# Performance work log

Measured on AMD Instinct MI355X. Metric: run time of the kernel, lower is better.

The kernel has to match this reference:

```python
import jax, jax.numpy as jnp
import numpy as np

SIGMA = 10
POPULATIONS = 2
LR = 0.001


def _normalize(L, prior):
    # clamp then normalize over populations (logsumexp across the population axis)
    O = L.shape[1]
    L = jnp.clip(L, -5.0, 0.0)
    lse = jax.nn.logsumexp(L.reshape(POPULATIONS, -1, O), axis=0)  # (in/P, O)
    L = L - jnp.tile(lse, (POPULATIONS, 1))
    prior = jnp.clip(prior, -5.0, 0.0)
    prior = prior - jax.nn.logsumexp(prior)
    return L, prior


def _forward(x, L, prior):
    B, T, IN = x.shape
    O = L.shape[1]
    L, prior = _normalize(L, prior)  # matches normalize_probs() in __init__

    # membrane potential: OR of spikes over trailing window of SIGMA steps
    xb = x.astype(bool)
    pot = xb
    for s in range(1, SIGMA):  # fixed small loop (sigma=10)
        pot = pot | jnp.pad(xb, ((0, 0), (s, 0), (0, 0)))[:, :T, :]

    tpre0 = jnp.full((B, IN), -T, dtype=jnp.int32)
    tpost0 = jnp.full((B, O), jnp.iinfo(jnp.int32).max, dtype=jnp.int32)
    base_key = jax.random.key(42)

    pot_T = jnp.transpose(pot, (1, 0, 2))  # (T,B,IN)
    x_T = jnp.transpose(xb, (1, 0, 2))

    def step(carry, inp):
        L, prior, tpre, tpost, t = carry
        pot_t, x_t = inp
        potf = pot_t.astype(L.dtype)
        logits = potf @ L + prior  # (B,O), logits <= 0 so exp is safe
        # torch: softmax(exp(logits)).multinomial == categorical with logits=exp(logits)
        key = jax.random.fold_in(base_key, t)
        widx = jax.random.categorical(key, jnp.exp(logits), axis=-1)  # (B,)
        win = jax.nn.one_hot(widx, O, dtype=L.dtype)
        # trace updates happen BEFORE STDP, as in the torch code
        tpre = jnp.where(x_t, 0, tpre - 1)
        tpost = jnp.where(win > 0, 0, tpost - 1)
        ltp = (tpre >= -SIGMA).astype(L.dtype)
        ltd = (tpre < -SIGMA).astype(L.dtype)
        post = (tpost < 0).astype(L.dtype)
        m_ltp = jnp.einsum('bi,bo->io', ltp, win) / B
        m_ltd = jnp.einsum('bi,bo->io', ltd, win) / B
        m_pp = jnp.einsum('bi,bo->io', potf, post) / B
        decay = (t + 1).astype(L.dtype)  # lr_decay_inverse starts at 1
        # dw = (5 e^{-L} - 1) * LTP.mean - LTD.mean - pre_post.mean ; LTD was negated
        dw = (5.0 * jnp.exp(-L) - 1.0) * m_ltp + m_ltd - m_pp
        L2 = L + (LR / decay) * dw
        wm = jnp.mean(win, axis=0)
        db = (-5.0 * prior - 1.0) * wm - (1.0 - wm)
        p2 = prior + (LR / decay) * db
        L2, p2 = _normalize(L2, p2)
        return (L2, p2, tpre, tpost, t + 1), None

    (Lf, pf, _, _, _), _ = jax.lax.scan(
        step, (L, prior, tpre0, tpost0, jnp.int32(0)), (pot_T, x_T))
    return jnp.concatenate([Lf.reshape(-1), pf])


def setup_inputs() -> dict:
    key = jax.random.key(0)
    k1, k2, k3 = jax.random.split(key, 3)
    B, T, IN, O = 256, 200, 1568, 100
    x = jax.random.randint(k1, (B, T, IN), 0, 2, dtype=jnp.int32)
    log_likelihood = jax.random.uniform(k2, (IN, O), dtype=jnp.float32) * -1.0 - 1.0
    log_prior = jax.random.uniform(k3, (O,), dtype=jnp.float32) * -1.0 - 1.0
    return {"x": x, "log_likelihood": log_likelihood, "log_prior": log_prior}


def reference(x, log_likelihood, log_prior):
    return _forward(x, log_likelihood, log_prior)
```

## Files before the change

kernel.cpp:

```cpp
#include <hip/hip_runtime.h>
#include <stdint.h>

#define BB 256
#define TT 200
#define INN 1568
#define OO 100
#define PAIRS 784
#define NHALF 12800
#define NBLK 240
#define UNITS 686
#define ROWSTRIDE (4 * INN)

typedef unsigned long long u64;
typedef __attribute__((ext_vector_type(4))) int v4i;

typedef const __attribute__((address_space(1))) uint32_t* gas_p;
typedef __attribute__((address_space(3))) uint32_t* las_p;
#define GLD16(g, l) __builtin_amdgcn_global_load_lds((gas_p)(g), (las_p)(l), 16, 0, 0)

__device__ __forceinline__ void tf_round(uint32_t& x0, uint32_t& x1, int r) {
    x0 += x1;
    x1 = (x1 << r) | (x1 >> (32 - r));
    x1 ^= x0;
}

__device__ __forceinline__ void threefry(uint32_t k0, uint32_t k1,
                                         uint32_t x0, uint32_t x1,
                                         uint32_t& o0, uint32_t& o1) {
    uint32_t k2 = k0 ^ k1 ^ 0x1BD11BDAu;
    x0 += k0; x1 += k1;
    tf_round(x0,x1,13); tf_round(x0,x1,15); tf_round(x0,x1,26); tf_round(x0,x1,6);
    x0 += k1; x1 += k2 + 1u;
    tf_round(x0,x1,17); tf_round(x0,x1,29); tf_round(x0,x1,16); tf_round(x0,x1,24);
    x0 += k2; x1 += k0 + 2u;
    tf_round(x0,x1,13); tf_round(x0,x1,15); tf_round(x0,x1,26); tf_round(x0,x1,6);
    x0 += k0; x1 += k1 + 3u;
    tf_round(x0,x1,17); tf_round(x0,x1,29); tf_round(x0,x1,16); tf_round(x0,x1,24);
    x0 += k1; x1 += k2 + 4u;
    tf_round(x0,x1,13); tf_round(x0,x1,15); tf_round(x0,x1,26); tf_round(x0,x1,6);
    o0 = x0 + k2; o1 = x1 + k0 + 5u;
}

struct FusedSM {
    u64 rows[8][16][64];
    u64 wp[8][8][128];
    u64 potC[8][2][8][10];
    u64 ltpC[8][2][8][10];
    uint32_t cntR[8][8][16];
};
struct FwSM { uint32_t wl32[TT * 65]; int fwl[BB]; };
union SMem { FusedSM f; FwSM w; };

__device__ __forceinline__ void gridsync(uint32_t* c) {
    __syncthreads();
    if (threadIdx.x == 0) {
        __threadfence();
        __hip_atomic_fetch_add(c, 1u, __ATOMIC_ACQ_REL, __HIP_MEMORY_SCOPE_AGENT);
        while (__hip_atomic_load(c, __ATOMIC_ACQUIRE, __HIP_MEMORY_SCOPE_AGENT)
               < (uint32_t)NBLK)
            __builtin_amdgcn_s_sleep(8);
        __threadfence();
    }
    __syncthreads();
}

__global__ __launch_bounds__(512, 1) void k_mono(
        const int* __restrict__ x,
        const float* __restrict__ L0,
        const float* __restrict__ p0arr,
        uint32_t* __restrict__ syncc,
        uint8_t* __restrict__ widx,
        uint32_t* __restrict__ cntg,
        u64* __restrict__ winbits,
        u64* __restrict__ postbits,
        u64* __restrict__ bitB,
        float* __restrict__ outL,
        float* __restrict__ outp) {
    __shared__ SMem sm;
    __shared__ uint32_t smclaim;
    const int tid = threadIdx.x;
    const int bid = blockIdx.x;

    {
        int idx = bid * 214 + tid;
        if (tid < 214 && idx < TT * BB) {
            int t = idx >> 8, b = idx & 255;
            uint32_t fk0, fk1;
            threefry(0u, 42u, 0u, (uint32_t)t, fk0, fk1);
            uint32_t bestkey = 0u;
            int bo = 0;
            int nbase = b * OO;
            for (int o = 0; o < OO; ++o) {
                uint32_t n = (uint32_t)(nbase + o);
                uint32_t lo = (n < NHALF) ? n : n - NHALF;
                uint32_t v0, v1;
                threefry(fk0, fk1, lo, lo + NHALF, v0, v1);
                uint32_t bits = (n < NHALF) ? v0 : v1;
                uint32_t key = bits >> 9;
                if (key > bestkey) { bestkey = key; bo = o; }
            }
            widx[idx] = (uint8_t)bo;
        }
    }
    gridsync(&syncc[0]);

    if (bid < 100) {
        const uint32_t* wsrc = (const uint32_t*)widx;
        for (int g = tid; g < TT * 64; g += 512)
            sm.w.wl32[(g >> 6) * 65 + (g & 63)] = wsrc[g];
        __syncthreads();
        int o = bid;
        if (tid < 64) {
            int f0 = 255, f1 = 255, f2 = 255, f3 = 255;
            for (int t = 0; t < TT; ++t) {
                uint32_t w4 = sm.w.wl32[t * 65 + tid];
                if (((w4      ) & 255u) == (uint32_t)o && f0 == 255) f0 = t;
                if (((w4 >>  8) & 255u) == (uint32_t)o && f1 == 255) f1 = t;
                if (((w4 >> 16) & 255u) == (uint32_t)o && f2 == 255) f2 = t;
                if (((w4 >> 24) & 255u) == (uint32_t)o && f3 == 255) f3 = t;
            }
            sm.w.fwl[4 * tid + 0] = f0; sm.w.fwl[4 * tid + 1] = f1;
            sm.w.fwl[4 * tid + 2] = f2; sm.w.fwl[4 * tid + 3] = f3;
        }
        __syncthreads();
        if (tid < TT) {
            int t = tid;
            u64 wbA[4], pbA[4];
            uint32_t c = 0;
            #pragma unroll
            for (int k = 0; k < 4; ++k) {
                u64 wacc = 0, pacc = 0;
                for (int q2 = 0; q2 < 16; ++q2) {
                    uint32_t w4 = sm.w.wl32[t * 65 + k * 16 + q2];
                    #pragma unroll
                    for (int j = 0; j < 4; ++j) {
                        int bl = q2 * 4 + j;
                        bool win = (((w4 >> (8 * j)) & 255u) == (uint32_t)o);
                        c += win ? 1u : 0u;
                        bool post = (sm.w.fwl[k * 64 + q2 * 4 + j] < t) && !win;
                        u64 bit = 1ull << bl;
                        if (win)  wacc |= bit;
                        if (post) pacc |= bit;
                    }
                }
                wbA[k] = wacc; pbA[k] = pacc;
            }
            size_t base = (size_t)(t * OO + o) * 4;
            #pragma unroll
            for (int k = 0; k < 4; ++k) {
                winbits[base + k] = wbA[k];
                postbits[base + k] = pbA[k];
            }
            cntg[t * OO + o] = c;
        }
        __syncthreads();
    }

    {
        const v4i* xp = (const v4i*)x;
        for (;;) {
            __syncthreads();
            if (tid == 0)
                smclaim = __hip_atomic_fetch_add(&syncc[2], 1u, __ATOMIC_RELAXED,
                                                 __HIP_MEMORY_SCOPE_AGENT);
            __syncthreads();
            uint32_t u = smclaim;
            if (u >= 200u) break;
            int wb = u & 3, tc = u >> 2;
            u64 acc[4][4];
            #pragma unroll
            for (int q = 0; q < 4; ++q)
                #pragma unroll
                for (int c = 0; c < 4; ++c) acc[q][c] = 0;
            bool x4 = (tid < 32);
            for (int blb = 0; blb < 64; blb += 4) {
                v4i v[4][3];
                v4i vt[4];
                #pragma unroll
                for (int s4 = 0; s4 < 4; ++s4) {
                    size_t base = ((size_t)((wb * 64 + blb + s4) * TT + tc * 4)) * 392;
                    #pragma unroll
                    for (int q = 0; q < 3; ++q)
                        v[s4][q] = __builtin_nontemporal_load(&xp[base + tid + q * 512]);
                    if (x4)
                        vt[s4] = __builtin_nontemporal_load(&xp[base + tid + 1536]);
                }
                #pragma unroll
                for (int s4 = 0; s4 < 4; ++s4) {
                    u64 bit = 1ull << (blb + s4);
                    #pragma unroll
                    for (int q = 0; q < 3; ++q) {
                        if (v[s4][q].x) acc[q][0] |= bit;
                        if (v[s4][q].y) acc[q][1] |= bit;
                        if (v[s4][q].z) acc[q][2] |= bit;
                        if (v[s4][q].w) acc[q][3] |= bit;
                    }
                    if (x4) {
                        if (vt[s4].x) acc[3][0] |= bit;
                        if (vt[s4].y) acc[3][1] |= bit;
                        if (vt[s4].z) acc[3][2] |= bit;
                        if (vt[s4].w) acc[3][3] |= bit;
                    }
                }
            }
            #pragma unroll
            for (int q = 0; q < 4; ++q) {
                if (q == 3 && !x4) continue;
                int p = tid + q * 512;
                int tp = (p >= 1176) ? 3 : (p >= 784) ? 2 : (p >= 392) ? 1 : 0;
                int iq = p - tp * 392;
                u64* dst = bitB + ((size_t)((tc * 4 + tp) * 4 + wb)) * INN + iq * 4;
                dst[0] = acc[q][0]; dst[1] = acc[q][1];
                dst[2] = acc[q][2]; dst[3] = acc[q][3];
            }
        }
    }
    gridsync(&syncc[1]);

    {
        const int wv = tid >> 6, lane = tid & 63;
        int u = bid + NBLK * wv;
        if (u > UNITS) return;
        if (u == UNITS) {
            int l = lane;
            bool has2 = (l + 64) < OO;
            float pa = p0arr[l];
            float pb = has2 ? p0arr[l + 64] : -1e30f;
            auto norm = [&]() {
                pa = fminf(fmaxf(pa, -5.0f), 0.0f);
                if (has2) pb = fminf(fmaxf(pb, -5.0f), 0.0f);
                float mx = has2 ? fmaxf(pa, pb) : pa;
                #pragma unroll
                for (int s = 32; s > 0; s >>= 1) mx = fmaxf(mx, __shfl_xor(mx, s, 64));
                float smv = expf(pa - mx) + (has2 ? expf(pb - mx) : 0.0f);
                #pragma unroll
                for (int s = 32; s > 0; s >>= 1) smv += __shfl_xor(smv, s, 64);
                float lse = logf(smv) + mx;
                pa -= lse;
                if (has2) pb -= lse;
            };
            norm();
            for (int t = 0; t < TT; ++t) {
                float eta = 0.001f / (float)(t + 1);
                float wma = (float)cntg[t * OO + l] * (1.0f / 256.0f);
                pa += eta * ((-5.0f * pa - 1.0f) * wma - (1.0f - wma));
                if (has2) {
                    float wmb = (float)cntg[t * OO + l + 64] * (1.0f / 256.0f);
                    pb += eta * ((-5.0f * pb - 1.0f) * wmb - (1.0f - wmb));
                }
                norm();
            }
            outp[l] = pa;
            if (has2) outp[l + 64] = pb;
            return;
        }

        const int pg = u % 98, og = u / 98;
        const int p0 = pg * 8, o0 = og * 16;
        const int pl = lane & 7, ol = lane >> 3;
        const int oA = o0 + ol, oB = oA + 8;
        const int i0 = p0 + pl, i1 = i0 + PAIRS;
        const bool actA = (oA < OO), actB = (oB < OO);

        const int e0 = (lane & 31) * 2;
        const int wk0 = e0 >> 3, wpl0 = e0 & 7;
        const u64* rowg = bitB + (size_t)((wk0 & 3) * INN + (wk0 >> 2) * PAIRS
                                          + p0 + wpl0);
        const int lw = lane & 31;
        const u64* wpg = (lane < 32) ? winbits : postbits;
        const bool wpact = (o0 + (lw >> 1)) < OO;
        const bool cntact = (lane < 8) && ((o0 + (lane & 3) * 4) < OO);

        auto issueG = [&](int G) {
            int r0 = 2 * G;
            {
                int rr = r0 + (lane >> 5); if (rr > TT - 1) rr = TT - 1;
                GLD16(rowg + (size_t)rr * ROWSTRIDE,
                      (las_p)&sm.f.rows[wv][r0 & 15][0]);
            }
            {
                int rr = r0; if (rr > TT - 1) rr = TT - 1;
                if (wpact)
                    GLD16(wpg + ((size_t)rr * OO + o0) * 4 + 2 * lw,
                          (las_p)&sm.f.wp[wv][r0 & 7][0]);
            }
            {
                int rr = r0 + 1; if (rr > TT - 1) rr = TT - 1;
                if (wpact)
                    GLD16(wpg + ((size_t)rr * OO + o0) * 4 + 2 * lw,
                          (las_p)&sm.f.wp[wv][(r0 + 1) & 7][0]);
            }
            {
                if (cntact) {
                    int rr = r0 + (lane >> 2); if (rr > TT - 1) rr = TT - 1;
                    GLD16(cntg + (size_t)rr * OO + o0 + (lane & 3) * 4,
                          (las_p)&sm.f.cntR[wv][r0 & 7][0]);
                }
            }
        };

        float aA = actA ? L0[(size_t)i0 * OO + oA] : -1.0f;
        float bA = actA ? L0[(size_t)i1 * OO + oA] : -1.0f;
        float aB = actB ? L0[(size_t)i0 * OO + oB] : -1.0f;
        float bB = actB ? L0[(size_t)i1 * OO + oB] : -1.0f;
        {
            aA = fminf(fmaxf(aA, -5.0f), 0.0f);
            bA = fminf(fmaxf(bA, -5.0f), 0.0f);
            float m = fmaxf(aA, bA), mn = fminf(aA, bA);
            float lse = __logf(1.0f + __expf(mn - m)) + m;
            aA -= lse; bA -= lse;
            aB = fminf(fmaxf(aB, -5.0f), 0.0f);
            bB = fminf(fmaxf(bB, -5.0f), 0.0f);
            float m2 = fmaxf(aB, bB), mn2 = fminf(aB, bB);
            float lse2 = __logf(1.0f + __expf(mn2 - m2)) + m2;
            aB -= lse2; bB -= lse2;
        }

        auto chainstep = [&](int t, int sp) {
            int s = t & 7;
            const u64* wpS = &sm.f.wp[wv][s][0];
            const u64* P = sm.f.potC[wv][sp][pl];
            const u64* Lt = sm.f.ltpC[wv][sp][pl];
            u64 P0 = P[0], P1 = P[1], P2 = P[2], P3 = P[3];
            u64 P4 = P[4], P5 = P[5], P6 = P[6], P7 = P[7];
            u64 Q0 = Lt[0], Q1 = Lt[1], Q2 = Lt[2], Q3 = Lt[3];
            u64 Q4 = Lt[4], Q5 = Lt[5], Q6 = Lt[6], Q7 = Lt[7];
            float eta = 0.001f / (float)(t + 1);
            {
                u64 W0 = wpS[ol*4+0], W1 = wpS[ol*4+1], W2 = wpS[ol*4+2], W3 = wpS[ol*4+3];
                u64 S0 = wpS[64+ol*4+0], S1 = wpS[64+ol*4+1], S2 = wpS[64+ol*4+2], S3 = wpS[64+ol*4+3];
                float cw = (float)sm.f.cntR[wv][s][ol];
                float lt0 = (float)(__popcll(Q0&W0)+__popcll(Q1&W1)+__popcll(Q2&W2)+__popcll(Q3&W3));
                float lt1 = (float)(__popcll(Q4&W0)+__popcll(Q5&W1)+__popcll(Q6&W2)+__popcll(Q7&W3));
                float pp0 = (float)(__popcll(P0&S0)+__popcll(P1&S1)+__popcll(P2&S2)+__popcll(P3&S3));
                float pp1 = (float)(__popcll(P4&S0)+__popcll(P5&S1)+__popcll(P6&S2)+__popcll(P7&S3));
                float dw0 = (5.0f*__expf(-aA) - 1.0f)*(lt0*(1.0f/256.0f))
                          + (cw - lt0 - pp0)*(1.0f/256.0f);
                float dw1 = (5.0f*__expf(-bA) - 1.0f)*(lt1*(1.0f/256.0f))
                          + (cw - lt1 - pp1)*(1.0f/256.0f);
                aA += eta*dw0; bA += eta*dw1;
                aA = fminf(fmaxf(aA,-5.0f),0.0f);
                bA = fminf(fmaxf(bA,-5.0f),0.0f);
                float m = fmaxf(aA,bA), mn = fminf(aA,bA);
                float lse = __logf(1.0f + __expf(mn-m)) + m;
                aA -= lse; bA -= lse;
            }
            {
                u64 W0 = wpS[(ol+8)*4+0], W1 = wpS[(ol+8)*4+1], W2 = wpS[(ol+8)*4+2], W3 = wpS[(ol+8)*4+3];
                u64 S0 = wpS[64+(ol+8)*4+0], S1 = wpS[64+(ol+8)*4+1], S2 = wpS[64+(ol+8)*4+2], S3 = wpS[64+(ol+8)*4+3];
                float cw = (float)sm.f.cntR[wv][s][ol+8];
                float lt0 = (float)(__popcll(Q0&W0)+__popcll(Q1&W1)+__popcll(Q2&W2)+__popcll(Q3&W3));
                float lt1 = (float)(__popcll(Q4&W0)+__popcll(Q5&W1)+__popcll(Q6&W2)+__popcll(Q7&W3));
                float pp0 = (float)(__popcll(P0&S0)+__popcll(P1&S1)+__popcll(P2&S2)+__popcll(P3&S3));
                float pp1 = (float)(__popcll(P4&S0)+__popcll(P5&S1)+__popcll(P6&S2)+__popcll(P7&S3));
                float dw0 = (5.0f*__expf(-aB) - 1.0f)*(lt0*(1.0f/256.0f))
                          + (cw - lt0 - pp0)*(1.0f/256.0f);
                float dw1 = (5.0f*__expf(-bB) - 1.0f)*(lt1*(1.0f/256.0f))
                          + (cw - lt1 - pp1)*(1.0f/256.0f);
                aB += eta*dw0; bB += eta*dw1;
                aB = fminf(fmaxf(aB,-5.0f),0.0f);
                bB = fminf(fmaxf(bB,-5.0f),0.0f);
                float m = fmaxf(aB,bB), mn = fminf(aB,bB);
                float lse = __logf(1.0f + __expf(mn-m)) + m;
                aB -= lse; bB -= lse;
            }
        };

        issueG(0);
        issueG(1);
        for (int I = 0; I < 100; ++I) {
            issueG(I + 2);
            asm volatile("s_waitcnt vmcnt(8)" ::: "memory");
            int b0 = 2 * I;
            u64 com = 0;
            #pragma unroll
            for (int j = 8; j >= 0; --j) {
                int r = b0 - j; r = (r < 0) ? 0 : r;
                com |= sm.f.rows[wv][r & 15][lane];
            }
            int r9 = b0 - 9;   r9 = (r9 < 0) ? 0 : r9;
            int r10 = b0 - 10; r10 = (r10 < 0) ? 0 : r10;
            u64 v9  = sm.f.rows[wv][r9 & 15][lane];
            u64 v10 = sm.f.rows[wv][r10 & 15][lane];
            u64 vt2 = sm.f.rows[wv][(b0 + 1) & 15][lane];
            u64 pot1 = com | v9;
            u64 pot2 = com | vt2;
            sm.f.potC[wv][0][lane & 7][lane >> 3] = pot1;
            sm.f.potC[wv][1][lane & 7][lane >> 3] = pot2;
            sm.f.ltpC[wv][0][lane & 7][lane >> 3] = pot1 | v10;
            sm.f.ltpC[wv][1][lane & 7][lane >> 3] = pot2 | v9;
            asm volatile("s_waitcnt lgkmcnt(0)" ::: "memory");
            chainstep(b0, 0);
            chainstep(b0 + 1, 1);
        }
        if (actA) {
            outL[(size_t)i0 * OO + oA] = aA;
            outL[(size_t)i1 * OO + oA] = bA;
        }
        if (actB) {
            outL[(size_t)i0 * OO + oB] = aB;
            outL[(size_t)i1 * OO + oB] = bB;
        }
    }
}

extern "C" void kernel_launch(void* const* d_in, const int* in_sizes, int n_in,
                              void* d_out, int out_size, void* d_ws, size_t ws_size,
                              hipStream_t stream) {
    const int*   x  = (const int*)d_in[0];
    const float* L0 = (const float*)d_in[1];
    const float* p0 = (const float*)d_in[2];
    float* out = (float*)d_out;

    char* ws = (char*)d_ws;
    size_t off = 0;
    auto alloc = [&](size_t bytes) -> void* {
        off = (off + 255) & ~(size_t)255;
        void* p = ws + off;
        off += bytes;
        return p;
    };
    uint32_t* syncc    = (uint32_t*)alloc(256);
    uint8_t*  widx     = (uint8_t*) alloc((size_t)TT * BB);
    uint32_t* cntg     = (uint32_t*)alloc((size_t)TT * OO * 4);
    u64*      winbits  = (u64*)     alloc((size_t)TT * OO * 4 * 8);
    u64*      postbits = (u64*)     alloc((size_t)TT * OO * 4 * 8);
    u64*      bitB     = (u64*)     alloc((size_t)TT * 4 * INN * 8);
    (void)ws_size;

    hipMemsetAsync(syncc, 0, 256, stream);
    hipLaunchKernelGGL(k_mono, dim3(NBLK), dim3(512), 0, stream,
                       x, L0, p0, syncc, widx, cntg, winbits, postbits, bitB,
                       out, out + (size_t)INN * OO);
}
```

Before: 689.1 us.

## Replace grid barriers with per-stage flags and specialize blocks by role

The two full-grid barriers are removed. Blocks are now split by role: blocks 172+ pack x into bitplanes and publish a per-time-chunk counter, blocks below 100 compute winners and win/post bitmasks and signal completion flags, and 4 waves per block run the STDP chains. Each chain waits only for the time chunks it needs before prefetching rows, with a deeper prefetch ring. This lets bit-packing overlap the chain recurrence instead of serializing phases, at the cost of fewer chain waves per block, spin-waiting, and a risk of deadlock if the producer blocks are not co-resident. The memset is also replaced by a tiny zeroing kernel.

```diff
diff --git a/kernel.cpp b/kernel.cpp
--- a/kernel.cpp
+++ b/kernel.cpp
@@ -8,8 +8,8 @@
 #define PAIRS 784
 #define NHALF 12800
 #define NBLK 240
-#define UNITS 686
 #define ROWSTRIDE (4 * INN)
+#define DW 4
 
 typedef unsigned long long u64;
 typedef __attribute__((ext_vector_type(4))) int v4i;
@@ -41,34 +41,30 @@
     o0 = x0 + k2; o1 = x1 + k0 + 5u;
 }
 
-struct FusedSM {
-    u64 rows[8][16][64];
-    u64 wp[8][8][128];
-    u64 potC[8][2][8][10];
-    u64 ltpC[8][2][8][10];
-    uint32_t cntR[8][8][16];
+#define F_CLAIM 0
+#define F_WIN   1
+#define F_FW    2
+#define F_TC    8
+
+__global__ __launch_bounds__(64) void k_zero(uint32_t* __restrict__ flags) {
+    flags[threadIdx.x] = 0;
+}
+
+struct ChSM {
+    u64 rows[DW][32][64];
+    u64 wp[DW][16][128];
+    u64 potC[DW][2][8][10];
+    u64 ltpC[DW][2][8][10];
+    uint32_t cntR[DW][16][16];
 };
 struct FwSM { uint32_t wl32[TT * 65]; int fwl[BB]; };
-union SMem { FusedSM f; FwSM w; };
-
-__device__ __forceinline__ void gridsync(uint32_t* c) {
-    __syncthreads();
-    if (threadIdx.x == 0) {
-        __threadfence();
-        __hip_atomic_fetch_add(c, 1u, __ATOMIC_ACQ_REL, __HIP_MEMORY_SCOPE_AGENT);
-        while (__hip_atomic_load(c, __ATOMIC_ACQUIRE, __HIP_MEMORY_SCOPE_AGENT)
-               < (uint32_t)NBLK)
-            __builtin_amdgcn_s_sleep(8);
-        __threadfence();
-    }
-    __syncthreads();
-}
+union SMem { ChSM c; FwSM w; };
 
 __global__ __launch_bounds__(512, 1) void k_mono(
         const int* __restrict__ x,
         const float* __restrict__ L0,
         const float* __restrict__ p0arr,
-        uint32_t* __restrict__ syncc,
+        uint32_t* __restrict__ flags,
         uint8_t* __restrict__ widx,
         uint32_t* __restrict__ cntg,
         u64* __restrict__ winbits,
@@ -81,92 +77,17 @@
     const int tid = threadIdx.x;
     const int bid = blockIdx.x;
 
-    {
-        int idx = bid * 214 + tid;
-        if (tid < 214 && idx < TT * BB) {
-            int t = idx >> 8, b = idx & 255;
-            uint32_t fk0, fk1;
-            threefry(0u, 42u, 0u, (uint32_t)t, fk0, fk1);
-            uint32_t bestkey = 0u;
-            int bo = 0;
-            int nbase = b * OO;
-            for (int o = 0; o < OO; ++o) {
-                uint32_t n = (uint32_t)(nbase + o);
-                uint32_t lo = (n < NHALF) ? n : n - NHALF;
-                uint32_t v0, v1;
-                threefry(fk0, fk1, lo, lo + NHALF, v0, v1);
-                uint32_t bits = (n < NHALF) ? v0 : v1;
-                uint32_t key = bits >> 9;
-                if (key > bestkey) { bestkey = key; bo = o; }
-            }
-            widx[idx] = (uint8_t)bo;
-        }
-    }
-    gridsync(&syncc[0]);
-
-    if (bid < 100) {
-        const uint32_t* wsrc = (const uint32_t*)widx;
-        for (int g = tid; g < TT * 64; g += 512)
-            sm.w.wl32[(g >> 6) * 65 + (g & 63)] = wsrc[g];
-        __syncthreads();
-        int o = bid;
-        if (tid < 64) {
-            int f0 = 255, f1 = 255, f2 = 255, f3 = 255;
-            for (int t = 0; t < TT; ++t) {
-                uint32_t w4 = sm.w.wl32[t * 65 + tid];
-                if (((w4      ) & 255u) == (uint32_t)o && f0 == 255) f0 = t;
-                if (((w4 >>  8) & 255u) == (uint32_t)o && f1 == 255) f1 = t;
-                if (((w4 >> 16) & 255u) == (uint32_t)o && f2 == 255) f2 = t;
-                if (((w4 >> 24) & 255u) == (uint32_t)o && f3 == 255) f3 = t;
-            }
-            sm.w.fwl[4 * tid + 0] = f0; sm.w.fwl[4 * tid + 1] = f1;
-            sm.w.fwl[4 * tid + 2] = f2; sm.w.fwl[4 * tid + 3] = f3;
-        }
-        __syncthreads();
-        if (tid < TT) {
-            int t = tid;
-            u64 wbA[4], pbA[4];
-            uint32_t c = 0;
-            #pragma unroll
-            for (int k = 0; k < 4; ++k) {
-                u64 wacc = 0, pacc = 0;
-                for (int q2 = 0; q2 < 16; ++q2) {
-                    uint32_t w4 = sm.w.wl32[t * 65 + k * 16 + q2];
-                    #pragma unroll
-                    for (int j = 0; j < 4; ++j) {
-                        int bl = q2 * 4 + j;
-                        bool win = (((w4 >> (8 * j)) & 255u) == (uint32_t)o);
-                        c += win ? 1u : 0u;
-                        bool post = (sm.w.fwl[k * 64 + q2 * 4 + j] < t) && !win;
-                        u64 bit = 1ull << bl;
-                        if (win)  wacc |= bit;
-                        if (post) pacc |= bit;
-                    }
-                }
-                wbA[k] = wacc; pbA[k] = pacc;
-            }
-            size_t base = (size_t)(t * OO + o) * 4;
-            #pragma unroll
-            for (int k = 0; k < 4; ++k) {
-                winbits[base + k] = wbA[k];
-                postbits[base + k] = pbA[k];
-            }
-            cntg[t * OO + o] = c;
-        }
-        __syncthreads();
-    }
-
-    {
+    if (bid >= 172) {
         const v4i* xp = (const v4i*)x;
         for (;;) {
             __syncthreads();
             if (tid == 0)
-                smclaim = __hip_atomic_fetch_add(&syncc[2], 1u, __ATOMIC_RELAXED,
-                                                 __HIP_MEMORY_SCOPE_AGENT);
+                smclaim = __hip_atomic_fetch_add(&flags[F_CLAIM], 1u,
+                              __ATOMIC_RELAXED, __HIP_MEMORY_SCOPE_AGENT);
             __syncthreads();
             uint32_t u = smclaim;
             if (u >= 200u) break;
-            int wb = u & 3, tc = u >> 2;
+            int wb = (int)(u & 3), tc = (int)(u >> 2);
             u64 acc[4][4];
             #pragma unroll
             for (int q = 0; q < 4; ++q)
@@ -213,194 +134,308 @@
                 dst[0] = acc[q][0]; dst[1] = acc[q][1];
                 dst[2] = acc[q][2]; dst[3] = acc[q][3];
             }
-        }
-    }
-    gridsync(&syncc[1]);
-
+            __syncthreads();
+            if (tid == 0) {
+                __threadfence();
+                __hip_atomic_fetch_add(&flags[F_TC + tc], 1u,
+                    __ATOMIC_ACQ_REL, __HIP_MEMORY_SCOPE_AGENT);
+            }
+        }
+        return;
+    }
+
+    if (bid < 100) {
+        {
+            int idx = bid * 512 + tid;
+            int t = idx >> 8, b = idx & 255;
+            uint32_t fk0, fk1;
+            threefry(0u, 42u, 0u, (uint32_t)t, fk0, fk1);
+            uint32_t bestkey = 0u;
+            int bo = 0;
+            int nbase = b * OO;
+            for (int o = 0; o < OO; ++o) {
+                uint32_t n = (uint32_t)(nbase + o);
+                uint32_t lo = (n < NHALF) ? n : n - NHALF;
+                uint32_t v0, v1;
+                threefry(fk0, fk1, lo, lo + NHALF, v0, v1);
+                uint32_t bits = (n < NHALF) ? v0 : v1;
+                uint32_t key = bits >> 9;
+                if (key > bestkey) { bestkey = key; bo = o; }
+            }
+            widx[idx] = (uint8_t)bo;
+        }
+        __syncthreads();
+        if (tid == 0) {
+            __threadfence();
+            __hip_atomic_fetch_add(&flags[F_WIN], 1u,
+                __ATOMIC_ACQ_REL, __HIP_MEMORY_SCOPE_AGENT);
+            while (__hip_atomic_load(&flags[F_WIN], __ATOMIC_ACQUIRE,
+                                     __HIP_MEMORY_SCOPE_AGENT) < 100u)
+                __builtin_amdgcn_s_sleep(8);
+            __threadfence();
+        }
+        __syncthreads();
+        {
+            const uint32_t* wsrc = (const uint32_t*)widx;
+            for (int g = tid; g < TT * 64; g += 512)
+                sm.w.wl32[(g >> 6) * 65 + (g & 63)] = wsrc[g];
+            __syncthreads();
+            int o = bid;
+            if (tid < 64) {
+                int f0 = 255, f1 = 255, f2 = 255, f3 = 255;
+                for (int t = 0; t < TT; ++t) {
+                    uint32_t w4 = sm.w.wl32[t * 65 + tid];
+                    if (((w4      ) & 255u) == (uint32_t)o && f0 == 255) f0 = t;
+                    if (((w4 >>  8) & 255u) == (uint32_t)o && f1 == 255) f1 = t;
+                    if (((w4 >> 16) & 255u) == (uint32_t)o && f2 == 255) f2 = t;
+                    if (((w4 >> 24) & 255u) == (uint32_t)o && f3 == 255) f3 = t;
+                }
+                sm.w.fwl[4 * tid + 0] = f0; sm.w.fwl[4 * tid + 1] = f1;
+                sm.w.fwl[4 * tid + 2] = f2; sm.w.fwl[4 * tid + 3] = f3;
+            }
+            __syncthreads();
+            if (tid < TT) {
+                int t = tid;
+                u64 wbA[4], pbA[4];
+                uint32_t c = 0;
+                #pragma unroll
+                for (int k = 0; k < 4; ++k) {
+                    u64 wacc = 0, pacc = 0;
+                    for (int q2 = 0; q2 < 16; ++q2) {
+                        uint32_t w4 = sm.w.wl32[t * 65 + k * 16 + q2];
+                        #pragma unroll
+                        for (int j = 0; j < 4; ++j) {
+                            int bl = q2 * 4 + j;
+                            bool win = (((w4 >> (8 * j)) & 255u) == (uint32_t)o);
+                            c += win ? 1u : 0u;
+                            bool post = (sm.w.fwl[k * 64 + q2 * 4 + j] < t) && !win;
+                            u64 bit = 1ull << bl;
+                            if (win)  wacc |= bit;
+                            if (post) pacc |= bit;
+                        }
+                    }
+                    wbA[k] = wacc; pbA[k] = pacc;
+                }
+                size_t base = (size_t)(t * OO + o) * 4;
+                #pragma unroll
+                for (int k = 0; k < 4; ++k) {
+                    winbits[base + k] = wbA[k];
+                    postbits[base + k] = pbA[k];
+                }
+                cntg[t * OO + o] = c;
+            }
+            __syncthreads();
+            if (tid == 0) {
+                __threadfence();
+                __hip_atomic_fetch_add(&flags[F_FW], 1u,
+                    __ATOMIC_ACQ_REL, __HIP_MEMORY_SCOPE_AGENT);
+            }
+        }
+    }
+
+    const int wv = tid >> 6, lane = tid & 63;
+    if (wv >= DW) return;
+    int u = bid * DW + wv;
+    if (u >= 687) return;
+
+    while (__hip_atomic_load(&flags[F_FW], __ATOMIC_ACQUIRE,
+                             __HIP_MEMORY_SCOPE_AGENT) < 100u)
+        __builtin_amdgcn_s_sleep(8);
+    __threadfence();
+
+    if (u == 686) {
+        int l = lane;
+        bool has2 = (l + 64) < OO;
+        float pa = p0arr[l];
+        float pb = has2 ? p0arr[l + 64] : -1e30f;
+        auto norm = [&]() {
+            pa = fminf(fmaxf(pa, -5.0f), 0.0f);
+            if (has2) pb = fminf(fmaxf(pb, -5.0f), 0.0f);
+            float mx = has2 ? fmaxf(pa, pb) : pa;
+            #pragma unroll
+            for (int s = 32; s > 0; s >>= 1) mx = fmaxf(mx, __shfl_xor(mx, s, 64));
+            float smv = expf(pa - mx) + (has2 ? expf(pb - mx) : 0.0f);
+            #pragma unroll
+            for (int s = 32; s > 0; s >>= 1) smv += __shfl_xor(smv, s, 64);
+            float lse = logf(smv) + mx;
+            pa -= lse;
+            if (has2) pb -= lse;
+        };
+        norm();
+        for (int t = 0; t < TT; ++t) {
+            float eta = 0.001f / (float)(t + 1);
+            float wma = (float)cntg[t * OO + l] * (1.0f / 256.0f);
+            pa += eta * ((-5.0f * pa - 1.0f) * wma - (1.0f - wma));
+            if (has2) {
+                float wmb = (float)cntg[t * OO + l + 64] * (1.0f / 256.0f);
+                pb += eta * ((-5.0f * pb - 1.0f) * wmb - (1.0f - wmb));
+            }
+            norm();
+        }
+        outp[l] = pa;
+        if (has2) outp[l + 64] = pb;
+        return;
+    }
+
+    const int pg = u % 98, og = u / 98;
+    const int p0 = pg * 8, o0 = og * 16;
+    const int pl = lane & 7, ol = lane >> 3;
+    const int oA = o0 + ol, oB = oA + 8;
+    const int i0 = p0 + pl, i1 = i0 + PAIRS;
+    const bool actA = (oA < OO), actB = (oB < OO);
+
+    const int e0 = (lane & 31) * 2;
+    const int wk0 = e0 >> 3, wpl0 = e0 & 7;
+    const u64* rowg = bitB + (size_t)((wk0 & 3) * INN + (wk0 >> 2) * PAIRS
+                                      + p0 + wpl0);
+    const int lw = lane & 31;
+    const u64* wpg = (lane < 32) ? winbits : postbits;
+    const bool wpact = (o0 + (lw >> 1)) < OO;
+    const bool cntact = (lane < 8) && ((o0 + (lane & 3) * 4) < OO);
+
+    int done_tc = -1;
+    auto wait_tc = [&](int need) {
+        if (done_tc >= need) return;
+        for (;;) {
+            uint32_t v = __hip_atomic_load(&flags[F_TC + done_tc + 1],
+                            __ATOMIC_ACQUIRE, __HIP_MEMORY_SCOPE_AGENT);
+            if (v >= 4u) { if (++done_tc >= need) break; }
+            else __builtin_amdgcn_s_sleep(4);
+        }
+        __threadfence();
+    };
+
+    auto issueG = [&](int G) {
+        int r0 = 2 * G;
+        {
+            int rr = r0 + (lane >> 5); if (rr > TT - 1) rr = TT - 1;
+            GLD16(rowg + (size_t)rr * ROWSTRIDE,
+                  (las_p)&sm.c.rows[wv][r0 & 31][0]);
+        }
+        {
+            int rr = r0; if (rr > TT - 1) rr = TT - 1;
+            if (wpact)
+                GLD16(wpg + ((size_t)rr * OO + o0) * 4 + 2 * lw,
+                      (las_p)&sm.c.wp[wv][r0 & 15][0]);
+        }
+        {
+            int rr = r0 + 1; if (rr > TT - 1) rr = TT - 1;
+            if (wpact)
+                GLD16(wpg + ((size_t)rr * OO + o0) * 4 + 2 * lw,
+                      (las_p)&sm.c.wp[wv][(r0 + 1) & 15][0]);
+        }
+        {
+            if (cntact) {
+                int rr = r0 + (lane >> 2); if (rr > TT - 1) rr = TT - 1;
+                GLD16(cntg + (size_t)rr * OO + o0 + (lane & 3) * 4,
+                      (las_p)&sm.c.cntR[wv][r0 & 15][0]);
+            }
+        }
+    };
+
+    float aA = actA ? L0[(size_t)i0 * OO + oA] : -1.0f;
+    float bA = actA ? L0[(size_t)i1 * OO + oA] : -1.0f;
+    float aB = actB ? L0[(size_t)i0 * OO + oB] : -1.0f;
+    float bB = actB ? L0[(size_t)i1 * OO + oB] : -1.0f;
     {
-        const int wv = tid >> 6, lane = tid & 63;
-        int u = bid + NBLK * wv;
-        if (u > UNITS) return;
-        if (u == UNITS) {
-            int l = lane;
-            bool has2 = (l + 64) < OO;
-            float pa = p0arr[l];
-            float pb = has2 ? p0arr[l + 64] : -1e30f;
-            auto norm = [&]() {
-                pa = fminf(fmaxf(pa, -5.0f), 0.0f);
-                if (has2) pb = fminf(fmaxf(pb, -5.0f), 0.0f);
-                float mx = has2 ? fmaxf(pa, pb) : pa;
-                #pragma unroll
-                for (int s = 32; s > 0; s >>= 1) mx = fmaxf(mx, __shfl_xor(mx, s, 64));
-                float smv = expf(pa - mx) + (has2 ? expf(pb - mx) : 0.0f);
-                #pragma unroll
-                for (int s = 32; s > 0; s >>= 1) smv += __shfl_xor(smv, s, 64);
-                float lse = logf(smv) + mx;
-                pa -= lse;
-                if (has2) pb -= lse;
-            };
-            norm();
-            for (int t = 0; t < TT; ++t) {
-                float eta = 0.001f / (float)(t + 1);
-                float wma = (float)cntg[t * OO + l] * (1.0f / 256.0f);
-                pa += eta * ((-5.0f * pa - 1.0f) * wma - (1.0f - wma));
-                if (has2) {
-                    float wmb = (float)cntg[t * OO + l + 64] * (1.0f / 256.0f);
-                    pb += eta * ((-5.0f * pb - 1.0f) * wmb - (1.0f - wmb));
-                }
-                norm();
-            }
-            outp[l] = pa;
-            if (has2) outp[l + 64] = pb;
-            return;
-        }
-
-        const int pg = u % 98, og = u / 98;
-        const int p0 = pg * 8, o0 = og * 16;
-        const int pl = lane & 7, ol = lane >> 3;
-        const int oA = o0 + ol, oB = oA + 8;
-        const int i0 = p0 + pl, i1 = i0 + PAIRS;
-        const bool actA = (oA < OO), actB = (oB < OO);
-
-        const int e0 = (lane & 31) * 2;
-        const int wk0 = e0 >> 3, wpl0 = e0 & 7;
-        const u64* rowg = bitB + (size_t)((wk0 & 3) * INN + (wk0 >> 2) * PAIRS
-                                          + p0 + wpl0);
-        const int lw = lane & 31;
-        const u64* wpg = (lane < 32) ? winbits : postbits;
-        const bool wpact = (o0 + (lw >> 1)) < OO;
-        const bool cntact = (lane < 8) && ((o0 + (lane & 3) * 4) < OO);
-
-        auto issueG = [&](int G) {
-            int r0 = 2 * G;
-            {
-                int rr = r0 + (lane >> 5); if (rr > TT - 1) rr = TT - 1;
-                GLD16(rowg + (size_t)rr * ROWSTRIDE,
-                      (las_p)&sm.f.rows[wv][r0 & 15][0]);
-            }
-            {
-                int rr = r0; if (rr > TT - 1) rr = TT - 1;
-                if (wpact)
-                    GLD16(wpg + ((size_t)rr * OO + o0) * 4 + 2 * lw,
-                          (las_p)&sm.f.wp[wv][r0 & 7][0]);
-            }
-            {
-                int rr = r0 + 1; if (rr > TT - 1) rr = TT - 1;
-                if (wpact)
-                    GLD16(wpg + ((size_t)rr * OO + o0) * 4 + 2 * lw,
-                          (las_p)&sm.f.wp[wv][(r0 + 1) & 7][0]);
-            }
-            {
-                if (cntact) {
-                    int rr = r0 + (lane >> 2); if (rr > TT - 1) rr = TT - 1;
-                    GLD16(cntg + (size_t)rr * OO + o0 + (lane & 3) * 4,
-                          (las_p)&sm.f.cntR[wv][r0 & 7][0]);
-                }
-            }
-        };
-
-        float aA = actA ? L0[(size_t)i0 * OO + oA] : -1.0f;
-        float bA = actA ? L0[(size_t)i1 * OO + oA] : -1.0f;
-        float aB = actB ? L0[(size_t)i0 * OO + oB] : -1.0f;
-        float bB = actB ? L0[(size_t)i1 * OO + oB] : -1.0f;
-        {
-            aA = fminf(fmaxf(aA, -5.0f), 0.0f);
-            bA = fminf(fmaxf(bA, -5.0f), 0.0f);
-            float m = fmaxf(aA, bA), mn = fminf(aA, bA);
-            float lse = __logf(1.0f + __expf(mn - m)) + m;
+        aA = fminf(fmaxf(aA, -5.0f), 0.0f);
+        bA = fminf(fmaxf(bA, -5.0f), 0.0f);
+        float m = fmaxf(aA, bA), mn = fminf(aA, bA);
+        float lse = __logf(1.0f + __expf(mn - m)) + m;
+        aA -= lse; bA -= lse;
+        aB = fminf(fmaxf(aB, -5.0f), 0.0f);
+        bB = fminf(fmaxf(bB, -5.0f), 0.0f);
+        float m2 = fmaxf(aB, bB), mn2 = fminf(aB, bB);
+        float lse2 = __logf(1.0f + __expf(mn2 - m2)) + m2;
+        aB -= lse2; bB -= lse2;
+    }
+
+    auto chainstep = [&](int t, int sp) {
+        int s = t & 15;
+        const u64* wpS = &sm.c.wp[wv][s][0];
+        const u64* P = sm.c.potC[wv][sp][pl];
+        const u64* Lt = sm.c.ltpC[wv][sp][pl];
+        u64 P0 = P[0], P1 = P[1], P2 = P[2], P3 = P[3];
+        u64 P4 = P[4], P5 = P[5], P6 = P[6], P7 = P[7];
+        u64 Q0 = Lt[0], Q1 = Lt[1], Q2 = Lt[2], Q3 = Lt[3];
+        u64 Q4 = Lt[4], Q5 = Lt[5], Q6 = Lt[6], Q7 = Lt[7];
+        float eta = 0.001f / (float)(t + 1);
+        {
+            u64 W0 = wpS[ol*4+0], W1 = wpS[ol*4+1], W2 = wpS[ol*4+2], W3 = wpS[ol*4+3];
+            u64 S0 = wpS[64+ol*4+0], S1 = wpS[64+ol*4+1], S2 = wpS[64+ol*4+2], S3 = wpS[64+ol*4+3];
+            float cw = (float)sm.c.cntR[wv][s][ol];
+            float lt0 = (float)(__popcll(Q0&W0)+__popcll(Q1&W1)+__popcll(Q2&W2)+__popcll(Q3&W3));
+            float lt1 = (float)(__popcll(Q4&W0)+__popcll(Q5&W1)+__popcll(Q6&W2)+__popcll(Q7&W3));
+            float pp0 = (float)(__popcll(P0&S0)+__popcll(P1&S1)+__popcll(P2&S2)+__popcll(P3&S3));
+            float pp1 = (float)(__popcll(P4&S0)+__popcll(P5&S1)+__popcll(P6&S2)+__popcll(P7&S3));
+            float dw0 = (5.0f*__expf(-aA) - 1.0f)*(lt0*(1.0f/256.0f))
+                      + (cw - lt0 - pp0)*(1.0f/256.0f);
+            float dw1 = (5.0f*__expf(-bA) - 1.0f)*(lt1*(1.0f/256.0f))
+                      + (cw - lt1 - pp1)*(1.0f/256.0f);
+            aA += eta*dw0; bA += eta*dw1;
+            aA = fminf(fmaxf(aA,-5.0f),0.0f);
+            bA = fminf(fmaxf(bA,-5.0f),0.0f);
+            float m = fmaxf(aA,bA), mn = fminf(aA,bA);
+            float lse = __logf(1.0f + __expf(mn-m)) + m;
             aA -= lse; bA -= lse;
-            aB = fminf(fmaxf(aB, -5.0f), 0.0f);
-            bB = fminf(fmaxf(bB, -5.0f), 0.0f);
-            float m2 = fmaxf(aB, bB), mn2 = fminf(aB, bB);
-            float lse2 = __logf(1.0f + __expf(mn2 - m2)) + m2;
-            aB -= lse2; bB -= lse2;
-        }
-
-        auto chainstep = [&](int t, int sp) {
-            int s = t & 7;
-            const u64* wpS = &sm.f.wp[wv][s][0];
-            const u64* P = sm.f.potC[wv][sp][pl];
-            const u64* Lt = sm.f.ltpC[wv][sp][pl];
-            u64 P0 = P[0], P1 = P[1], P2 = P[2], P3 = P[3];
-            u64 P4 = P[4], P5 = P[5], P6 = P[6], P7 = P[7];
-            u64 Q0 = Lt[0], Q1 = Lt[1], Q2 = Lt[2], Q3 = Lt[3];
-            u64 Q4 = Lt[4], Q5 = Lt[5], Q6 = Lt[6], Q7 = Lt[7];
-            float eta = 0.001f / (float)(t + 1);
-            {
-                u64 W0 = wpS[ol*4+0], W1 = wpS[ol*4+1], W2 = wpS[ol*4+2], W3 = wpS[ol*4+3];
-                u64 S0 = wpS[64+ol*4+0], S1 = wpS[64+ol*4+1], S2 = wpS[64+ol*4+2], S3 = wpS[64+ol*4+3];
-                float cw = (float)sm.f.cntR[wv][s][ol];
-                float lt0 = (float)(__popcll(Q0&W0)+__popcll(Q1&W1)+__popcll(Q2&W2)+__popcll(Q3&W3));
-                float lt1 = (float)(__popcll(Q4&W0)+__popcll(Q5&W1)+__popcll(Q6&W2)+__popcll(Q7&W3));
-                float pp0 = (float)(__popcll(P0&S0)+__popcll(P1&S1)+__popcll(P2&S2)+__popcll(P3&S3));
-                float pp1 = (float)(__popcll(P4&S0)+__popcll(P5&S1)+__popcll(P6&S2)+__popcll(P7&S3));
-                float dw0 = (5.0f*__expf(-aA) - 1.0f)*(lt0*(1.0f/256.0f))
-                          + (cw - lt0 - pp0)*(1.0f/256.0f);
-                float dw1 = (5.0f*__expf(-bA) - 1.0f)*(lt1*(1.0f/256.0f))
-                          + (cw - lt1 - pp1)*(1.0f/256.0f);
-                aA += eta*dw0; bA += eta*dw1;
-                aA = fminf(fmaxf(aA,-5.0f),0.0f);
-                bA = fminf(fmaxf(bA,-5.0f),0.0f);
-                float m = fmaxf(aA,bA), mn = fminf(aA,bA);
-                float lse = __logf(1.0f + __expf(mn-m)) + m;
-                aA -= lse; bA -= lse;
-            }
-            {
-                u64 W0 = wpS[(ol+8)*4+0], W1 = wpS[(ol+8)*4+1], W2 = wpS[(ol+8)*4+2], W3 = wpS[(ol+8)*4+3];
-                u64 S0 = wpS[64+(ol+8)*4+0], S1 = wpS[64+(ol+8)*4+1], S2 = wpS[64+(ol+8)*4+2], S3 = wpS[64+(ol+8)*4+3];
-                float cw = (float)sm.f.cntR[wv][s][ol+8];
-                float lt0 = (float)(__popcll(Q0&W0)+__popcll(Q1&W1)+__popcll(Q2&W2)+__popcll(Q3&W3));
-                float lt1 = (float)(__popcll(Q4&W0)+__popcll(Q5&W1)+__popcll(Q6&W2)+__popcll(Q7&W3));
-                float pp0 = (float)(__popcll(P0&S0)+__popcll(P1&S1)+__popcll(P2&S2)+__popcll(P3&S3));
-                float pp1 = (float)(__popcll(P4&S0)+__popcll(P5&S1)+__popcll(P6&S2)+__popcll(P7&S3));
-                float dw0 = (5.0f*__expf(-aB) - 1.0f)*(lt0*(1.0f/256.0f))
-                          + (cw - lt0 - pp0)*(1.0f/256.0f);
-                float dw1 = (5.0f*__expf(-bB) - 1.0f)*(lt1*(1.0f/256.0f))
-                          + (cw - lt1 - pp1)*(1.0f/256.0f);
-                aB += eta*dw0; bB += eta*dw1;
-                aB = fminf(fmaxf(aB,-5.0f),0.0f);
-                bB = fminf(fmaxf(bB,-5.0f),0.0f);
-                float m = fmaxf(aB,bB), mn = fminf(aB,bB);
-                float lse = __logf(1.0f + __expf(mn-m)) + m;
-                aB -= lse; bB -= lse;
-            }
-        };
-
-        issueG(0);
-        issueG(1);
-        for (int I = 0; I < 100; ++I) {
-            issueG(I + 2);
-            asm volatile("s_waitcnt vmcnt(8)" ::: "memory");
-            int b0 = 2 * I;
-            u64 com = 0;
-            #pragma unroll
-            for (int j = 8; j >= 0; --j) {
-                int r = b0 - j; r = (r < 0) ? 0 : r;
-                com |= sm.f.rows[wv][r & 15][lane];
-            }
-            int r9 = b0 - 9;   r9 = (r9 < 0) ? 0 : r9;
-            int r10 = b0 - 10; r10 = (r10 < 0) ? 0 : r10;
-            u64 v9  = sm.f.rows[wv][r9 & 15][lane];
-            u64 v10 = sm.f.rows[wv][r10 & 15][lane];
-            u64 vt2 = sm.f.rows[wv][(b0 + 1) & 15][lane];
-            u64 pot1 = com | v9;
-            u64 pot2 = com | vt2;
-            sm.f.potC[wv][0][lane & 7][lane >> 3] = pot1;
-            sm.f.potC[wv][1][lane & 7][lane >> 3] = pot2;
-            sm.f.ltpC[wv][0][lane & 7][lane >> 3] = pot1 | v10;
-            sm.f.ltpC[wv][1][lane & 7][lane >> 3] = pot2 | v9;
-            asm volatile("s_waitcnt lgkmcnt(0)" ::: "memory");
-            chainstep(b0, 0);
-            chainstep(b0 + 1, 1);
-        }
-        if (actA) {
-            outL[(size_t)i0 * OO + oA] = aA;
-            outL[(size_t)i1 * OO + oA] = bA;
-        }
-        if (actB) {
-            outL[(size_t)i0 * OO + oB] = aB;
-            outL[(size_t)i1 * OO + oB] = bB;
-        }
+        }
+        {
+            u64 W0 = wpS[(ol+8)*4+0], W1 = wpS[(ol+8)*4+1], W2 = wpS[(ol+8)*4+2], W3 = wpS[(ol+8)*4+3];
+            u64 S0 = wpS[64+(ol+8)*4+0], S1 = wpS[64+(ol+8)*4+1], S2 = wpS[64+(ol+8)*4+2], S3 = wpS[64+(ol+8)*4+3];
+            float cw = (float)sm.c.cntR[wv][s][ol+8];
+            float lt0 = (float)(__popcll(Q0&W0)+__popcll(Q1&W1)+__popcll(Q2&W2)+__popcll(Q3&W3));
+            float lt1 = (float)(__popcll(Q4&W0)+__popcll(Q5&W1)+__popcll(Q6&W2)+__popcll(Q7&W3));
+            float pp0 = (float)(__popcll(P0&S0)+__popcll(P1&S1)+__popcll(P2&S2)+__popcll(P3&S3));
+            float pp1 = (float)(__popcll(P4&S0)+__popcll(P5&S1)+__popcll(P6&S2)+__popcll(P7&S3));
+            float dw0 = (5.0f*__expf(-aB) - 1.0f)*(lt0*(1.0f/256.0f))
+                      + (cw - lt0 - pp0)*(1.0f/256.0f);
+            float dw1 = (5.0f*__expf(-bB) - 1.0f)*(lt1*(1.0f/256.0f))
+                      + (cw - lt1 - pp1)*(1.0f/256.0f);
+            aB += eta*dw0; bB += eta*dw1;
+            aB = fminf(fmaxf(aB,-5.0f),0.0f);
+            bB = fminf(fmaxf(bB,-5.0f),0.0f);
+            float m = fmaxf(aB,bB), mn = fminf(aB,bB);
+            float lse = __logf(1.0f + __expf(mn-m)) + m;
+            aB -= lse; bB -= lse;
+        }
+    };
+
+    wait_tc(1);
+    issueG(0); issueG(1); issueG(2); issueG(3);
+    for (int I = 0; I < 100; ++I) {
+        int rmax = 2 * I + 9; if (rmax > TT - 1) rmax = TT - 1;
+        wait_tc(rmax >> 2);
+        issueG(I + 4);
+        asm volatile("s_waitcnt vmcnt(16)" ::: "memory");
+        int b0 = 2 * I;
+        u64 com = 0;
+        #pragma unroll
+        for (int j = 8; j >= 0; --j) {
+            int r = b0 - j; r = (r < 0) ? 0 : r;
+            com |= sm.c.rows[wv][r & 31][lane];
+        }
+        int r9 = b0 - 9;   r9 = (r9 < 0) ? 0 : r9;
+        int r10 = b0 - 10; r10 = (r10 < 0) ? 0 : r10;
+        u64 v9  = sm.c.rows[wv][r9 & 31][lane];
+        u64 v10 = sm.c.rows[wv][r10 & 31][lane];
+        u64 vt2 = sm.c.rows[wv][(b0 + 1) & 31][lane];
+        u64 pot1 = com | v9;
+        u64 pot2 = com | vt2;
+        sm.c.potC[wv][0][lane & 7][lane >> 3] = pot1;
+        sm.c.potC[wv][1][lane & 7][lane >> 3] = pot2;
+        sm.c.ltpC[wv][0][lane & 7][lane >> 3] = pot1 | v10;
+        sm.c.ltpC[wv][1][lane & 7][lane >> 3] = pot2 | v9;
+        asm volatile("s_waitcnt lgkmcnt(0)" ::: "memory");
+        chainstep(b0, 0);
+        chainstep(b0 + 1, 1);
+    }
+    if (actA) {
+        outL[(size_t)i0 * OO + oA] = aA;
+        outL[(size_t)i1 * OO + oA] = bA;
+    }
+    if (actB) {
+        outL[(size_t)i0 * OO + oB] = aB;
+        outL[(size_t)i1 * OO + oB] = bB;
     }
 }
 
@@ -420,7 +455,7 @@
         off += bytes;
         return p;
     };
-    uint32_t* syncc    = (uint32_t*)alloc(256);
+    uint32_t* flags    = (uint32_t*)alloc(256);
     uint8_t*  widx     = (uint8_t*) alloc((size_t)TT * BB);
     uint32_t* cntg     = (uint32_t*)alloc((size_t)TT * OO * 4);
     u64*      winbits  = (u64*)     alloc((size_t)TT * OO * 4 * 8);
@@ -428,8 +463,8 @@
     u64*      bitB     = (u64*)     alloc((size_t)TT * 4 * INN * 8);
     (void)ws_size;
 
-    hipMemsetAsync(syncc, 0, 256, stream);
+    hipLaunchKernelGGL(k_zero, dim3(1), dim3(64), 0, stream, flags);
     hipLaunchKernelGGL(k_mono, dim3(NBLK), dim3(512), 0, stream,
-                       x, L0, p0, syncc, widx, cntg, winbits, postbits, bitB,
+                       x, L0, p0, flags, widx, cntg, winbits, postbits, bitB,
                        out, out + (size_t)INN * OO);
 }
```

Result: slower. 1.677 ms (+143.4%).
